# Performance work log

Measured on AMD Instinct MI355X. Metric: run time of the kernel, lower is better.

## Reference

```python
import jax, jax.numpy as jnp
import numpy as np

NUM_CAPSULE = 16
DIM_CAPSULE = 32
ROUTINGS = 4
EPS = 1e-07


def squash(x, axis=-1):
    # NOTE: faithful to the source: x / sqrt(sum(x^2) + eps) (unit-norm style),
    # NOT the standard Hinton squash.
    s2 = jnp.sum(x * x, axis=axis, keepdims=True)
    return x / jnp.sqrt(s2 + EPS)


def setup_inputs() -> dict:
    key = jax.random.key(0)
    k1, k2 = jax.random.split(key)
    B, N_in, D_in = 128, 1024, 256
    x = jax.random.normal(k1, (B, N_in, D_in), dtype=jnp.float32)
    # xavier_normal over (1, D_in, NUM_CAPSULE*DIM_CAPSULE)
    fan_in, fan_out = D_in, NUM_CAPSULE * DIM_CAPSULE
    std = np.sqrt(2.0 / (fan_in + fan_out))
    W = jax.random.normal(k2, (1, D_in, NUM_CAPSULE * DIM_CAPSULE), dtype=jnp.float32) * std
    return {"x": x, "W": W}


def reference(x, W):
    B, N_in, _ = x.shape
    # u_hat: [B, N_in, num_cap*dim_cap] -> [B, num_cap, N_in, dim_cap]
    u_hat = jnp.matmul(x, W[0])
    u_hat = u_hat.reshape(B, N_in, NUM_CAPSULE, DIM_CAPSULE).transpose(0, 2, 1, 3)

    b = jnp.zeros((B, NUM_CAPSULE, N_in), dtype=u_hat.dtype)
    outputs = None
    for i in range(ROUTINGS):
        # torch permutes to softmax over the num_capsule axis; equivalent to axis=1 here
        c = jax.nn.softmax(b, axis=1)                      # [B, num_cap, N_in]
        outputs = squash(jnp.einsum('bij,bijk->bik', c, u_hat))  # [B, num_cap, dim_cap]
        if i < ROUTINGS - 1:
            b = jnp.einsum('bik,bijk->bij', outputs, u_hat)
    return outputs
```

## Files before the change

### kernel.cpp

```cpp
#include <hip/hip_runtime.h>
#include <hip/hip_bf16.h>

typedef unsigned int u32;
typedef float f32x4 __attribute__((ext_vector_type(4)));
typedef __bf16 bf16x8 __attribute__((ext_vector_type(8)));

#define BATCH 128
#define NIN   1024
#define DIN   256
#define NC    16
#define DC    32
#define JC    64
#define NCHUNK 16

__device__ __forceinline__ u32 bfround(u32 ua){ return (ua + 0x7fffu + ((ua >> 16) & 1u)) >> 16; }
__device__ __forceinline__ u32 pack2(float a, float b){
    return (bfround(__float_as_uint(a)) & 0xffffu) | (bfround(__float_as_uint(b)) << 16);
}
__device__ __forceinline__ bf16x8 ldfrag(const u32* p){
    return __builtin_bit_cast(bf16x8, *(const uint4*)p);
}

__global__ __launch_bounds__(256) void k_colsum(const float* __restrict__ x, float* __restrict__ ysum){
    int chunk = blockIdx.x, b = blockIdx.y, t = threadIdx.x;
    const float* xb = x + ((size_t)b * NIN + chunk * 128) * DIN + t;
    float a = 0.f;
    #pragma unroll 4
    for (int j = 0; j < 128; j++) a += xb[j * DIN];
    atomicAdd(&ysum[b * DIN + t], a);
}

__global__ __launch_bounds__(256) void k_route(const float* __restrict__ x, const float* __restrict__ z,
                                               float* __restrict__ y){
    __shared__ __align__(16) u32 xl [64 * 128];
    __shared__ __align__(16) u32 xtl[256 * 32];
    __shared__ __align__(16) u32 zl [16 * 128];
    __shared__ __align__(16) u32 cl [16 * 32];
    const int t = threadIdx.x;
    const int bidx = blockIdx.y, chunk = blockIdx.x;
    const int lane = t & 63, wv = t >> 6;
    const int l15 = lane & 15, q = lane >> 4;

    {
        const float4* xg = (const float4*)(x + ((size_t)bidx * NIN + chunk * JC) * DIN);
        #pragma unroll
        for (int m = 0; m < 8; m++){
            int p = t + 256 * m;
            float4 a = xg[2 * p], c4 = xg[2 * p + 1];
            int j = p >> 5, w = 4 * (p & 31);
            uint4 W4;
            W4.x = pack2(a.x, a.y);  W4.y = pack2(a.z, a.w);
            W4.z = pack2(c4.x, c4.y); W4.w = pack2(c4.z, c4.w);
            *(uint4*)&xl[j * 128 + ((w + 4 * j) & 127)] = W4;
        }
        const float4* zg = (const float4*)(z + (size_t)bidx * NC * DIN);
        #pragma unroll
        for (int m = 0; m < 2; m++){
            int p = t + 256 * m;
            float4 a = zg[2 * p], c4 = zg[2 * p + 1];
            int i = p >> 5, w = 4 * (p & 31);
            uint4 W4;
            W4.x = pack2(a.x, a.y);  W4.y = pack2(a.z, a.w);
            W4.z = pack2(c4.x, c4.y); W4.w = pack2(c4.z, c4.w);
            *(uint4*)&zl[i * 128 + ((w + 4 * i) & 127)] = W4;
        }
    }
    __syncthreads();

    f32x4 acc1 = {0.f, 0.f, 0.f, 0.f};
    {
        int jr = wv * 16 + l15;
        #pragma unroll
        for (int ks = 0; ks < 8; ks++){
            int w = ks * 16 + q * 4;
            bf16x8 a = ldfrag(&xl[jr  * 128 + ((w + 4 * jr)  & 127)]);
            bf16x8 b = ldfrag(&zl[l15 * 128 + ((w + 4 * l15) & 127)]);
            acc1 = __builtin_amdgcn_mfma_f32_16x16x32_bf16(a, b, acc1, 0, 0, 0);
        }
    }
    float crs[4];
    #pragma unroll
    for (int r = 0; r < 4; r++){
        float v = acc1[r];
        float mx = v;
        mx = fmaxf(mx, __shfl_xor(mx, 1)); mx = fmaxf(mx, __shfl_xor(mx, 2));
        mx = fmaxf(mx, __shfl_xor(mx, 4)); mx = fmaxf(mx, __shfl_xor(mx, 8));
        float e = __expf(v - mx);
        float s = e;
        s += __shfl_xor(s, 1); s += __shfl_xor(s, 2);
        s += __shfl_xor(s, 4); s += __shfl_xor(s, 8);
        crs[r] = e / s;
    }
    {
        int jp0 = wv * 8 + q * 2;
        uint2 cw; cw.x = pack2(crs[0], crs[1]); cw.y = pack2(crs[2], crs[3]);
        *(uint2*)&cl[l15 * 32 + ((jp0 + 4 * l15) & 31)] = cw;
    }
    {
        int w = t & 127, jph = (t >> 7) * 16;
        int d0 = 2 * w, d1 = 2 * w + 1;
        #pragma unroll
        for (int g = 0; g < 4; g++){
            u32 o0[4], o1[4];
            #pragma unroll
            for (int e = 0; e < 4; e++){
                int jp = jph + g * 4 + e;
                u32 r0 = xl[(2 * jp)     * 128 + ((w + 8 * jp)     & 127)];
                u32 r1 = xl[(2 * jp + 1) * 128 + ((w + 8 * jp + 4) & 127)];
                o0[e] = (r0 & 0xffffu) | (r1 << 16);
                o1[e] = (r0 >> 16)     | (r1 & 0xffff0000u);
            }
            int jp0 = jph + g * 4;
            *(uint4*)&xtl[d0 * 32 + ((jp0 + 4 * d0) & 31)] = make_uint4(o0[0], o0[1], o0[2], o0[3]);
            *(uint4*)&xtl[d1 * 32 + ((jp0 + 4 * d1) & 31)] = make_uint4(o1[0], o1[1], o1[2], o1[3]);
        }
    }
    __syncthreads();

    {
        bf16x8 a0 = ldfrag(&cl[l15 * 32 + ((     q * 4 + 4 * l15) & 31)]);
        bf16x8 a1 = ldfrag(&cl[l15 * 32 + ((16 + q * 4 + 4 * l15) & 31)]);
        float* yb = y + (size_t)bidx * NC * DIN;
        #pragma unroll
        for (int nt = 0; nt < 4; nt++){
            int d = (wv * 4 + nt) * 16 + l15;
            f32x4 acc2 = {0.f, 0.f, 0.f, 0.f};
            bf16x8 b0 = ldfrag(&xtl[d * 32 + ((     q * 4 + 4 * d) & 31)]);
            acc2 = __builtin_amdgcn_mfma_f32_16x16x32_bf16(a0, b0, acc2, 0, 0, 0);
            bf16x8 b1 = ldfrag(&xtl[d * 32 + ((16 + q * 4 + 4 * d) & 31)]);
            acc2 = __builtin_amdgcn_mfma_f32_16x16x32_bf16(a1, b1, acc2, 0, 0, 0);
            #pragma unroll
            for (int r = 0; r < 4; r++)
                atomicAdd(&yb[(q * 4 + r) * DIN + d], acc2[r]);
        }
    }
}

__global__ __launch_bounds__(64) void k_out(const float* __restrict__ y, int ybs, int yis,
                                            const float* __restrict__ W, float* __restrict__ z,
                                            float* __restrict__ out, int final){
    __shared__ __align__(16) float ol[DC];
    const int i = blockIdx.x, b = blockIdx.y, t = threadIdx.x;
    const int col = t & 31, half = t >> 5;
    const float* yrow = y + (size_t)b * ybs + i * yis;
    const float* wc = W + i * DC + col;
    float s = 0.f;
    #pragma unroll 4
    for (int dd = 0; dd < 128; dd++){
        int d = half * 128 + dd;
        s += yrow[d] * wc[(size_t)d * 512];
    }
    s += __shfl_xor(s, 32);
    float v = s * s;
    v += __shfl_xor(v, 16); v += __shfl_xor(v, 8); v += __shfl_xor(v, 4);
    v += __shfl_xor(v, 2);  v += __shfl_xor(v, 1);
    float o = s / sqrtf(v + 1e-7f);
    if (final){
        if (t < 32) out[((size_t)b * NC + i) * DC + col] = o;
        return;
    }
    if (t < 32) ol[col] = o;
    __syncthreads();
    float4 ov[8];
    #pragma unroll
    for (int k4 = 0; k4 < 8; k4++) ov[k4] = *(const float4*)&ol[k4 * 4];
    float za[4];
    #pragma unroll
    for (int dd = 0; dd < 4; dd++){
        int d = t * 4 + dd;
        const float4* wr = (const float4*)(W + (size_t)d * 512 + i * DC);
        float acc = 0.f;
        #pragma unroll
        for (int k4 = 0; k4 < 8; k4++){
            float4 wv4 = wr[k4];
            acc += wv4.x * ov[k4].x + wv4.y * ov[k4].y + wv4.z * ov[k4].z + wv4.w * ov[k4].w;
        }
        za[dd] = acc;
    }
    *(float4*)&z[((size_t)b * NC + i) * DIN + t * 4] = make_float4(za[0], za[1], za[2], za[3]);
}

extern "C" void kernel_launch(void* const* d_in, const int* in_sizes, int n_in,
                              void* d_out, int out_size, void* d_ws, size_t ws_size,
                              hipStream_t stream){
    const float* x = (const float*)d_in[0];
    const float* W = (const float*)d_in[1];
    float* out = (float*)d_out;
    float* f = (float*)d_ws;
    float* ysum = f;
    float* y    = f + 32768;
    float* z    = f + 32768 + 524288;

    hipMemsetAsync(ysum, 0, 32768 * sizeof(float), stream);
    k_colsum<<<dim3(8, BATCH), 256, 0, stream>>>(x, ysum);
    k_out<<<dim3(NC, BATCH), 64, 0, stream>>>(ysum, DIN, 0, W, z, out, 0);
    for (int it = 1; it < 4; it++){
        hipMemsetAsync(y, 0, (size_t)BATCH * NC * DIN * sizeof(float), stream);
        k_route<<<dim3(NCHUNK, BATCH), 256, 0, stream>>>(x, z, y);
        k_out<<<dim3(NC, BATCH), 64, 0, stream>>>(y, NC * DIN, DIN, W, z, out, it == 3 ? 1 : 0);
    }
}
```

Before: 397.5 us.

## Precompute bf16 copy of x and W, fuse squash/z into per-batch kernel

Adds a prepass that converts x to bf16 once, alongside the column sum, so each of the three routing iterations reads half the bytes instead of re-reading and re-packing fp32 x. W is converted to two bf16 layouts, and the per-capsule output kernel is replaced by one 512-thread block per batch. That block computes squash and writes z directly in MFMA fragment order, which k_route loads straight into registers. In exchange it adds an extra write of x in bf16, rounds W and z to bf16 with some accuracy risk, and uses more workspace.

Result: faster. 382.4 us (-3.8%).

```diff
diff --git a/kernel.cpp b/kernel.cpp
--- a/kernel.cpp
+++ b/kernel.cpp
@@ -10,9 +10,10 @@
 #define DIN   256
 #define NC    16
 #define DC    32
-#define JC    64
-#define NCHUNK 16
-
+#define NCOL  512
+
+__device__ __forceinline__ float bflo(u32 v){ return __uint_as_float(v << 16); }
+__device__ __forceinline__ float bfhi(u32 v){ return __uint_as_float(v & 0xffff0000u); }
 __device__ __forceinline__ u32 bfround(u32 ua){ return (ua + 0x7fffu + ((ua >> 16) & 1u)) >> 16; }
 __device__ __forceinline__ u32 pack2(float a, float b){
     return (bfround(__float_as_uint(a)) & 0xffffu) | (bfround(__float_as_uint(b)) << 16);
@@ -21,48 +22,114 @@
     return __builtin_bit_cast(bf16x8, *(const uint4*)p);
 }
 
-__global__ __launch_bounds__(256) void k_colsum(const float* __restrict__ x, float* __restrict__ ysum){
-    int chunk = blockIdx.x, b = blockIdx.y, t = threadIdx.x;
-    const float* xb = x + ((size_t)b * NIN + chunk * 128) * DIN + t;
-    float a = 0.f;
+__global__ __launch_bounds__(256) void k_wconv(const float* __restrict__ W,
+                                               u32* __restrict__ Wt, u32* __restrict__ Wb){
+    int id = blockIdx.x * 256 + threadIdx.x;
+    {   int n = id >> 7, dp = id & 127;
+        Wt[id] = pack2(W[(size_t)(2 * dp) * NCOL + n], W[(size_t)(2 * dp + 1) * NCOL + n]); }
+    {   int d = id >> 8, np = id & 255;
+        Wb[id] = pack2(W[(size_t)d * NCOL + 2 * np], W[(size_t)d * NCOL + 2 * np + 1]); }
+}
+
+__global__ __launch_bounds__(256) void k_pre(const float* __restrict__ x, u32* __restrict__ xbf,
+                                             float* __restrict__ yd0){
+    const int jb = blockIdx.x, b = blockIdx.y, t = threadIdx.x;
+    const size_t base = (size_t)b * NIN + jb * 64;
+    const float4* xg = (const float4*)(x + base * DIN);
+    #pragma unroll
+    for (int m = 0; m < 16; m++){
+        int id = t + 256 * m;
+        int j = id >> 6, dq = id & 63;
+        float4 v = xg[id];
+        uint2 p; p.x = pack2(v.x, v.y); p.y = pack2(v.z, v.w);
+        *(uint2*)&xbf[(base + j) * 128 + dq * 2] = p;
+    }
+    float s = 0.f;
     #pragma unroll 4
-    for (int j = 0; j < 128; j++) a += xb[j * DIN];
-    atomicAdd(&ysum[b * DIN + t], a);
-}
-
-__global__ __launch_bounds__(256) void k_route(const float* __restrict__ x, const float* __restrict__ z,
-                                               float* __restrict__ y){
+    for (int j = 0; j < 64; j++) s += x[(base + j) * DIN + t];
+    atomicAdd(&yd0[b * DIN + t], s);
+}
+
+__global__ __launch_bounds__(512) void k_sz(const float* __restrict__ ydIn, int ybs, int yis,
+                                            const u32* __restrict__ Wt, const u32* __restrict__ Wb,
+                                            uint4* __restrict__ zf, float* __restrict__ out, int final){
+    __shared__ float ydl[NC * DIN];
+    __shared__ float ol[NCOL];
+    const int b = blockIdx.x, t = threadIdx.x;
+    #pragma unroll
+    for (int m = 0; m < 8; m++){
+        int idx = t + 512 * m;
+        int i = idx >> 8, d = idx & 255;
+        ydl[idx] = ydIn[(size_t)b * ybs + i * yis + d];
+    }
+    __syncthreads();
+    const int n = t, i = n >> 5;
+    const uint4* wr = (const uint4*)&Wt[n * 128];
+    const float2* yr = (const float2*)&ydl[i * DIN];
+    float s = 0.f;
+    #pragma unroll
+    for (int w4 = 0; w4 < 32; w4++){
+        uint4 u = wr[w4];
+        float2 q0 = yr[4 * w4], q1 = yr[4 * w4 + 1], q2 = yr[4 * w4 + 2], q3 = yr[4 * w4 + 3];
+        s += bflo(u.x) * q0.x + bfhi(u.x) * q0.y + bflo(u.y) * q1.x + bfhi(u.y) * q1.y
+           + bflo(u.z) * q2.x + bfhi(u.z) * q2.y + bflo(u.w) * q3.x + bfhi(u.w) * q3.y;
+    }
+    float v = s * s;
+    v += __shfl_xor(v, 1); v += __shfl_xor(v, 2); v += __shfl_xor(v, 4);
+    v += __shfl_xor(v, 8); v += __shfl_xor(v, 16);
+    float o = s / sqrtf(v + 1e-7f);
+    if (final){ out[(size_t)b * NCOL + n] = o; return; }
+    ol[n] = o;
+    __syncthreads();
+    const int i2 = t >> 5, dp0 = 4 * (t & 31);
+    float oc[DC];
+    #pragma unroll
+    for (int e = 0; e < 8; e++) *(float4*)&oc[4 * e] = *(const float4*)&ol[i2 * DC + 4 * e];
+    u32 zw[4];
+    #pragma unroll
+    for (int e = 0; e < 4; e++){
+        int d0 = 2 * (dp0 + e);
+        float za[2];
+        #pragma unroll
+        for (int h = 0; h < 2; h++){
+            const uint4* wbr = (const uint4*)&Wb[(size_t)(d0 + h) * 256 + i2 * 16];
+            float acc = 0.f;
+            #pragma unroll
+            for (int g = 0; g < 4; g++){
+                uint4 u = wbr[g];
+                acc += bflo(u.x) * oc[8*g+0] + bfhi(u.x) * oc[8*g+1]
+                     + bflo(u.y) * oc[8*g+2] + bfhi(u.y) * oc[8*g+3]
+                     + bflo(u.z) * oc[8*g+4] + bfhi(u.z) * oc[8*g+5]
+                     + bflo(u.w) * oc[8*g+6] + bfhi(u.w) * oc[8*g+7];
+            }
+            za[h] = acc;
+        }
+        zw[e] = pack2(za[0], za[1]);
+    }
+    int ks = dp0 >> 4, q = (dp0 >> 2) & 3;
+    zf[(size_t)b * 512 + ks * 64 + q * 16 + i2] = make_uint4(zw[0], zw[1], zw[2], zw[3]);
+}
+
+__global__ __launch_bounds__(256) void k_route(const u32* __restrict__ xbf, const uint4* __restrict__ zf,
+                                               float* __restrict__ yd){
     __shared__ __align__(16) u32 xl [64 * 128];
     __shared__ __align__(16) u32 xtl[256 * 32];
-    __shared__ __align__(16) u32 zl [16 * 128];
     __shared__ __align__(16) u32 cl [16 * 32];
-    const int t = threadIdx.x;
-    const int bidx = blockIdx.y, chunk = blockIdx.x;
+    const int t = threadIdx.x, chunk = blockIdx.x, b = blockIdx.y;
     const int lane = t & 63, wv = t >> 6;
     const int l15 = lane & 15, q = lane >> 4;
 
-    {
-        const float4* xg = (const float4*)(x + ((size_t)bidx * NIN + chunk * JC) * DIN);
+    uint4 zfr[8];
+    #pragma unroll
+    for (int ks = 0; ks < 8; ks++) zfr[ks] = zf[(size_t)b * 512 + ks * 64 + lane];
+
+    {
+        const uint4* ug = (const uint4*)&xbf[((size_t)b * NIN + chunk * 64) * 128];
         #pragma unroll
         for (int m = 0; m < 8; m++){
-            int p = t + 256 * m;
-            float4 a = xg[2 * p], c4 = xg[2 * p + 1];
-            int j = p >> 5, w = 4 * (p & 31);
-            uint4 W4;
-            W4.x = pack2(a.x, a.y);  W4.y = pack2(a.z, a.w);
-            W4.z = pack2(c4.x, c4.y); W4.w = pack2(c4.z, c4.w);
-            *(uint4*)&xl[j * 128 + ((w + 4 * j) & 127)] = W4;
-        }
-        const float4* zg = (const float4*)(z + (size_t)bidx * NC * DIN);
-        #pragma unroll
-        for (int m = 0; m < 2; m++){
-            int p = t + 256 * m;
-            float4 a = zg[2 * p], c4 = zg[2 * p + 1];
-            int i = p >> 5, w = 4 * (p & 31);
-            uint4 W4;
-            W4.x = pack2(a.x, a.y);  W4.y = pack2(a.z, a.w);
-            W4.z = pack2(c4.x, c4.y); W4.w = pack2(c4.z, c4.w);
-            *(uint4*)&zl[i * 128 + ((w + 4 * i) & 127)] = W4;
+            int id = t + 256 * m;
+            int j = id >> 5, w4 = id & 31;
+            *(uint4*)&xl[j * 128 + ((4 * w4 + 4 * j) & 127)] = ug[id];
         }
     }
     __syncthreads();
@@ -72,10 +139,8 @@
         int jr = wv * 16 + l15;
         #pragma unroll
         for (int ks = 0; ks < 8; ks++){
-            int w = ks * 16 + q * 4;
-            bf16x8 a = ldfrag(&xl[jr  * 128 + ((w + 4 * jr)  & 127)]);
-            bf16x8 b = ldfrag(&zl[l15 * 128 + ((w + 4 * l15) & 127)]);
-            acc1 = __builtin_amdgcn_mfma_f32_16x16x32_bf16(a, b, acc1, 0, 0, 0);
+            bf16x8 a = ldfrag(&xl[jr * 128 + ((ks * 16 + q * 4 + 4 * jr) & 127)]);
+            acc1 = __builtin_amdgcn_mfma_f32_16x16x32_bf16(a, __builtin_bit_cast(bf16x8, zfr[ks]), acc1, 0, 0, 0);
         }
     }
     float crs[4];
@@ -86,10 +151,10 @@
         mx = fmaxf(mx, __shfl_xor(mx, 1)); mx = fmaxf(mx, __shfl_xor(mx, 2));
         mx = fmaxf(mx, __shfl_xor(mx, 4)); mx = fmaxf(mx, __shfl_xor(mx, 8));
         float e = __expf(v - mx);
-        float s = e;
-        s += __shfl_xor(s, 1); s += __shfl_xor(s, 2);
-        s += __shfl_xor(s, 4); s += __shfl_xor(s, 8);
-        crs[r] = e / s;
+        float sm = e;
+        sm += __shfl_xor(sm, 1); sm += __shfl_xor(sm, 2);
+        sm += __shfl_xor(sm, 4); sm += __shfl_xor(sm, 8);
+        crs[r] = e / sm;
     }
     {
         int jp0 = wv * 8 + q * 2;
@@ -120,7 +185,7 @@
     {
         bf16x8 a0 = ldfrag(&cl[l15 * 32 + ((     q * 4 + 4 * l15) & 31)]);
         bf16x8 a1 = ldfrag(&cl[l15 * 32 + ((16 + q * 4 + 4 * l15) & 31)]);
-        float* yb = y + (size_t)bidx * NC * DIN;
+        float* yb = yd + (size_t)b * NC * DIN;
         #pragma unroll
         for (int nt = 0; nt < 4; nt++){
             int d = (wv * 4 + nt) * 16 + l15;
@@ -136,50 +201,6 @@
     }
 }
 
-__global__ __launch_bounds__(64) void k_out(const float* __restrict__ y, int ybs, int yis,
-                                            const float* __restrict__ W, float* __restrict__ z,
-                                            float* __restrict__ out, int final){
-    __shared__ __align__(16) float ol[DC];
-    const int i = blockIdx.x, b = blockIdx.y, t = threadIdx.x;
-    const int col = t & 31, half = t >> 5;
-    const float* yrow = y + (size_t)b * ybs + i * yis;
-    const float* wc = W + i * DC + col;
-    float s = 0.f;
-    #pragma unroll 4
-    for (int dd = 0; dd < 128; dd++){
-        int d = half * 128 + dd;
-        s += yrow[d] * wc[(size_t)d * 512];
-    }
-    s += __shfl_xor(s, 32);
-    float v = s * s;
-    v += __shfl_xor(v, 16); v += __shfl_xor(v, 8); v += __shfl_xor(v, 4);
-    v += __shfl_xor(v, 2);  v += __shfl_xor(v, 1);
-    float o = s / sqrtf(v + 1e-7f);
-    if (final){
-        if (t < 32) out[((size_t)b * NC + i) * DC + col] = o;
-        return;
-    }
-    if (t < 32) ol[col] = o;
-    __syncthreads();
-    float4 ov[8];
-    #pragma unroll
-    for (int k4 = 0; k4 < 8; k4++) ov[k4] = *(const float4*)&ol[k4 * 4];
-    float za[4];
-    #pragma unroll
-    for (int dd = 0; dd < 4; dd++){
-        int d = t * 4 + dd;
-        const float4* wr = (const float4*)(W + (size_t)d * 512 + i * DC);
-        float acc = 0.f;
-        #pragma unroll
-        for (int k4 = 0; k4 < 8; k4++){
-            float4 wv4 = wr[k4];
-            acc += wv4.x * ov[k4].x + wv4.y * ov[k4].y + wv4.z * ov[k4].z + wv4.w * ov[k4].w;
-        }
-        za[dd] = acc;
-    }
-    *(float4*)&z[((size_t)b * NC + i) * DIN + t * 4] = make_float4(za[0], za[1], za[2], za[3]);
-}
-
 extern "C" void kernel_launch(void* const* d_in, const int* in_sizes, int n_in,
                               void* d_out, int out_size, void* d_ws, size_t ws_size,
                               hipStream_t stream){
@@ -187,16 +208,20 @@
     const float* W = (const float*)d_in[1];
     float* out = (float*)d_out;
     float* f = (float*)d_ws;
-    float* ysum = f;
-    float* y    = f + 32768;
-    float* z    = f + 32768 + 524288;
-
-    hipMemsetAsync(ysum, 0, 32768 * sizeof(float), stream);
-    k_colsum<<<dim3(8, BATCH), 256, 0, stream>>>(x, ysum);
-    k_out<<<dim3(NC, BATCH), 64, 0, stream>>>(ysum, DIN, 0, W, z, out, 0);
+    float* yd0 = f;
+    float* yd  = f + 32768;
+    u32*   Wt  = (u32*)(f + 557056);
+    u32*   Wb  = (u32*)(f + 622592);
+    uint4* zfb = (uint4*)(f + 688128);
+    u32*   xbf = (u32*)(f + 950272);
+
+    hipMemsetAsync(yd0, 0, 32768 * sizeof(float), stream);
+    k_wconv<<<256, 256, 0, stream>>>(W, Wt, Wb);
+    k_pre<<<dim3(16, BATCH), 256, 0, stream>>>(x, xbf, yd0);
+    k_sz<<<BATCH, 512, 0, stream>>>(yd0, DIN, 0, Wt, Wb, zfb, out, 0);
     for (int it = 1; it < 4; it++){
-        hipMemsetAsync(y, 0, (size_t)BATCH * NC * DIN * sizeof(float), stream);
-        k_route<<<dim3(NCHUNK, BATCH), 256, 0, stream>>>(x, z, y);
-        k_out<<<dim3(NC, BATCH), 64, 0, stream>>>(y, NC * DIN, DIN, W, z, out, it == 3 ? 1 : 0);
-    }
-}
+        hipMemsetAsync(yd, 0, (size_t)BATCH * NC * DIN * sizeof(float), stream);
+        k_route<<<dim3(16, BATCH), 256, 0, stream>>>(xbf, zfb, yd);
+        k_sz<<<BATCH, 512, 0, stream>>>(yd, NC * DIN, DIN, Wt, Wb, zfb, out, it == 3 ? 1 : 0);
+    }
+}
```
